# Optimization experiments

Measured on AMD Instinct MI355X. Metric: run time of the kernel, lower is better.

Reference implementation:

```python
import jax, jax.numpy as jnp
import numpy as np

N_NODES = 500_000
N_OUTDIM = 256
HIDDEN = 512
N_REPRE = 128
NUM_GRAPHS = 1024  # = max(graph_idx) + 1 by construction


def setup_inputs() -> dict:
    key = jax.random.key(0)
    ks = jax.random.split(key, 8)
    node_states = jax.random.normal(ks[0], (N_NODES, N_OUTDIM), dtype=jnp.float32)
    graph_idx = jnp.sort(jax.random.randint(ks[1], (N_NODES,), 0, NUM_GRAPHS, dtype=jnp.int64))
    s1 = 1.0 / np.sqrt(N_OUTDIM)
    s2 = 1.0 / np.sqrt(HIDDEN)
    W1 = jax.random.uniform(ks[2], (N_OUTDIM, HIDDEN), jnp.float32, -s1, s1)
    b1 = jax.random.uniform(ks[3], (HIDDEN,), jnp.float32, -s1, s1)
    W2 = jax.random.uniform(ks[4], (HIDDEN, HIDDEN), jnp.float32, -s2, s2)
    b2 = jax.random.uniform(ks[5], (HIDDEN,), jnp.float32, -s2, s2)
    W3 = jax.random.uniform(ks[6], (HIDDEN, N_REPRE), jnp.float32, -s2, s2)
    b3 = jax.random.uniform(ks[7], (N_REPRE,), jnp.float32, -s2, s2)
    return {"node_states": node_states, "graph_idx": graph_idx,
            "W1": W1, "b1": b1, "W2": W2, "b2": b2, "W3": W3, "b3": b3}


def reference(node_states, graph_idx, W1, b1, W2, b2, W3, b3):
    # 3-layer MLP: Linear -> ReLU -> Linear -> ReLU -> Linear
    h = jax.nn.relu(node_states @ W1 + b1)          # [N, HIDDEN]
    h = jax.nn.relu(h @ W2 + b2)                     # [N, HIDDEN]
    y = h @ W3 + b3                                  # [N, N_REPRE]
    # gated = sigmoid(y) * y  (SiLU)
    g = jax.nn.sigmoid(y) * y
    # scatter-add per-graph segment sum -> [NUM_GRAPHS, N_REPRE]
    return jax.ops.segment_sum(g, graph_idx, num_segments=NUM_GRAPHS)
```

## Files before the change

### kernel.cpp

```cpp
#include <hip/hip_runtime.h>
#include <stdint.h>


typedef short bf16x8 __attribute__((ext_vector_type(8)));
typedef float f32x4  __attribute__((ext_vector_type(4)));

#define N_NODES   500000
#define BM        32
#define N_BLOCKS  (N_NODES / BM)
#define N_GRAPHS  1024
#define N_OUT     128

#define W1P_ELEMS (256*512)
#define W2P_ELEMS (512*512)
#define W3P_ELEMS (512*128)
#define W2P_OFF   (W1P_ELEMS)
#define W3P_OFF   (W1P_ELEMS + W2P_ELEMS)
#define PREPACK_THREADS ((W1P_ELEMS + W2P_ELEMS + W3P_ELEMS) / 8)

__device__ __forceinline__ short f2bf(float x) {
    uint32_t u = __float_as_uint(x);
    u += 0x7fffu + ((u >> 16) & 1u);
    return (short)(u >> 16);
}

__global__ void prepack_weights(const float* __restrict__ W1,
                                const float* __restrict__ W2,
                                const float* __restrict__ W3,
                                short* __restrict__ wp) {
    int tid = blockIdx.x * blockDim.x + threadIdx.x;
    if (tid >= PREPACK_THREADS) return;
    const float* src; int N, kmask, kshift, dstoff, local;
    if (tid < 16384) {
        src = W1; N = 512; kmask = 7;  kshift = 3; dstoff = 0;       local = tid;
    } else if (tid < 49152) {
        src = W2; N = 512; kmask = 15; kshift = 4; dstoff = W2P_OFF; local = tid - 16384;
    } else {
        src = W3; N = 128; kmask = 15; kshift = 4; dstoff = W3P_OFF; local = tid - 49152;
    }
    const int lane = local & 63;
    const int tile = local >> 6;
    const int kt = tile & kmask;
    const int nt = tile >> kshift;
    const int k0 = kt * 32 + (lane >> 4) * 8;
    const int n  = nt * 16 + (lane & 15);
    const float* s = src + (size_t)k0 * N + n;
    union { bf16x8 v; short e[8]; } u;
#pragma unroll
    for (int j = 0; j < 8; ++j) u.e[j] = f2bf(s[(size_t)j * N]);
    *((bf16x8*)(wp + dstoff) + local) = u.v;
}

__launch_bounds__(256, 2)
__global__ void fused_mlp(const float* __restrict__ X,
                          const int*   __restrict__ gidx,
                          const short* __restrict__ wp,
                          const float* __restrict__ b1,
                          const float* __restrict__ b2,
                          const float* __restrict__ b3,
                          float* __restrict__ out) {
    __shared__ __align__(16) char lds[65536];
    char* R0 = lds;
    char* R1 = lds + 32768;

    const int t    = threadIdx.x;
    const int lane = t & 63;
    const int wave = t >> 6;
    const int q    = lane >> 4;
    const int l15  = lane & 15;
    const int64_t rowBase = (int64_t)blockIdx.x * BM;

    const f32x4 zero4 = {0.f, 0.f, 0.f, 0.f};

    {
        const int m  = t >> 3;
        const int s  = t & 7;
        const int sw = m & 7;
        const float* xr = X + (rowBase + m) * 256;
#pragma unroll
        for (int i = 0; i < 8; ++i) {
            const int col = (s + 8 * i) * 4;
            const float4 f = *(const float4*)(xr + col);
            short4 h;
            h.x = f2bf(f.x); h.y = f2bf(f.y); h.z = f2bf(f.z); h.w = f2bf(f.w);
            const int c = col >> 3;
            const int off = m * 512 + ((c ^ sw) << 4) + ((col >> 2) & 1) * 8;
            *(short4*)(R0 + off) = h;
        }
    }
    __syncthreads();

    {
        f32x4 acc[2][8];
#pragma unroll
        for (int rt = 0; rt < 2; ++rt)
#pragma unroll
            for (int c8 = 0; c8 < 8; ++c8) acc[rt][c8] = zero4;
        const bf16x8* wB = (const bf16x8*)wp;
        for (int kt = 0; kt < 8; ++kt) {
            bf16x8 a[2];
#pragma unroll
            for (int rt = 0; rt < 2; ++rt) {
                const int m = rt * 16 + l15;
                const int c = kt * 4 + q;
                a[rt] = *(const bf16x8*)(R0 + m * 512 + ((c ^ (m & 7)) << 4));
            }
#pragma unroll
            for (int c8 = 0; c8 < 8; ++c8) {
                const int ct = wave * 8 + c8;
                const bf16x8 b = wB[(ct * 8 + kt) * 64 + lane];
                acc[0][c8] = __builtin_amdgcn_mfma_f32_16x16x32_bf16(a[0], b, acc[0][c8], 0, 0, 0);
                acc[1][c8] = __builtin_amdgcn_mfma_f32_16x16x32_bf16(a[1], b, acc[1][c8], 0, 0, 0);
            }
        }
#pragma unroll
        for (int c8 = 0; c8 < 8; ++c8) {
            const int n = (wave * 8 + c8) * 16 + l15;
            const float bias = b1[n];
            const int cg = n >> 3;
            const int nl = n & 7;
#pragma unroll
            for (int rt = 0; rt < 2; ++rt)
#pragma unroll
                for (int r = 0; r < 4; ++r) {
                    const int m = rt * 16 + q * 4 + r;
                    float v = acc[rt][c8][r] + bias;
                    v = fmaxf(v, 0.f);
                    *(short*)(R1 + m * 1024 + ((cg ^ (m & 7)) << 4) + nl * 2) = f2bf(v);
                }
        }
    }
    __syncthreads();

    {
        f32x4 acc[2][8];
#pragma unroll
        for (int rt = 0; rt < 2; ++rt)
#pragma unroll
            for (int c8 = 0; c8 < 8; ++c8) acc[rt][c8] = zero4;
        const bf16x8* wB = (const bf16x8*)wp + (W2P_OFF >> 3);
        for (int kt = 0; kt < 16; ++kt) {
            bf16x8 a[2];
#pragma unroll
            for (int rt = 0; rt < 2; ++rt) {
                const int m = rt * 16 + l15;
                const int c = kt * 4 + q;
                a[rt] = *(const bf16x8*)(R1 + m * 1024 + ((c ^ (m & 7)) << 4));
            }
#pragma unroll
            for (int c8 = 0; c8 < 8; ++c8) {
                const int ct = wave * 8 + c8;
                const bf16x8 b = wB[(ct * 16 + kt) * 64 + lane];
                acc[0][c8] = __builtin_amdgcn_mfma_f32_16x16x32_bf16(a[0], b, acc[0][c8], 0, 0, 0);
                acc[1][c8] = __builtin_amdgcn_mfma_f32_16x16x32_bf16(a[1], b, acc[1][c8], 0, 0, 0);
            }
        }
#pragma unroll
        for (int c8 = 0; c8 < 8; ++c8) {
            const int n = (wave * 8 + c8) * 16 + l15;
            const float bias = b2[n];
            const int cg = n >> 3;
            const int nl = n & 7;
#pragma unroll
            for (int rt = 0; rt < 2; ++rt)
#pragma unroll
                for (int r = 0; r < 4; ++r) {
                    const int m = rt * 16 + q * 4 + r;
                    float v = acc[rt][c8][r] + bias;
                    v = fmaxf(v, 0.f);
                    *(short*)(R0 + m * 1024 + ((cg ^ (m & 7)) << 4) + nl * 2) = f2bf(v);
                }
        }
    }
    __syncthreads();

    {
        f32x4 acc[2][2];
#pragma unroll
        for (int rt = 0; rt < 2; ++rt)
#pragma unroll
            for (int c2 = 0; c2 < 2; ++c2) acc[rt][c2] = zero4;
        const bf16x8* wB = (const bf16x8*)wp + (W3P_OFF >> 3);
        for (int kt = 0; kt < 16; ++kt) {
            bf16x8 a[2];
#pragma unroll
            for (int rt = 0; rt < 2; ++rt) {
                const int m = rt * 16 + l15;
                const int c = kt * 4 + q;
                a[rt] = *(const bf16x8*)(R0 + m * 1024 + ((c ^ (m & 7)) << 4));
            }
#pragma unroll
            for (int c2 = 0; c2 < 2; ++c2) {
                const int ct = wave * 2 + c2;
                const bf16x8 b = wB[(ct * 16 + kt) * 64 + lane];
                acc[0][c2] = __builtin_amdgcn_mfma_f32_16x16x32_bf16(a[0], b, acc[0][c2], 0, 0, 0);
                acc[1][c2] = __builtin_amdgcn_mfma_f32_16x16x32_bf16(a[1], b, acc[1][c2], 0, 0, 0);
            }
        }
        float* yl = (float*)R1;
#pragma unroll
        for (int c2 = 0; c2 < 2; ++c2) {
            const int n = (wave * 2 + c2) * 16 + l15;
            const float bias = b3[n];
#pragma unroll
            for (int rt = 0; rt < 2; ++rt)
#pragma unroll
                for (int r = 0; r < 4; ++r) {
                    const int m = rt * 16 + q * 4 + r;
                    const float yv = acc[rt][c2][r] + bias;
                    const float gv = yv / (1.f + __expf(-yv));
                    yl[m * 132 + n] = gv;
                }
        }
    }
    __syncthreads();

    {
        int* gs = (int*)R0;
        if (t < BM) gs[t] = gidx[rowBase + t];
        __syncthreads();
        const int col = t & 127;
        const int r0  = (t >> 7) * 16;
        const float* yl = (const float*)R1;
        int   gprev = gs[r0];
        float acc   = 0.f;
        for (int r = r0; r < r0 + 16; ++r) {
            const int gr = gs[r];
            if (gr != gprev) {
                atomicAdd(out + gprev * N_OUT + col, acc);
                acc = 0.f;
                gprev = gr;
            }
            acc += yl[r * 132 + col];
        }
        atomicAdd(out + gprev * N_OUT + col, acc);
    }
}

extern "C" void kernel_launch(void* const* d_in, const int* in_sizes, int n_in,
                              void* d_out, int out_size, void* d_ws, size_t ws_size,
                              hipStream_t stream) {
    const float* X    = (const float*)d_in[0];
    const int*   gidx = (const int*)  d_in[1];
    const float* W1   = (const float*)d_in[2];
    const float* b1   = (const float*)d_in[3];
    const float* W2   = (const float*)d_in[4];
    const float* b2   = (const float*)d_in[5];
    const float* W3   = (const float*)d_in[6];
    const float* b3   = (const float*)d_in[7];
    float* out = (float*)d_out;
    short* wp  = (short*)d_ws;

    hipMemsetAsync(d_out, 0, sizeof(float) * N_GRAPHS * N_OUT, stream);

    prepack_weights<<<PREPACK_THREADS / 256, 256, 0, stream>>>(W1, W2, W3, wp);

    fused_mlp<<<N_BLOCKS, 256, 0, stream>>>(X, gidx, wp, b1, b2, b3, out);
}
```

Before: 1.189 ms.

## Double row tile to 64 with 8 waves and re-tiled weight layout

Raises the per-block row tile from 32 to 64 rows and the block from 256 to 512 threads. Each wave now computes 4 row tiles by 4 column tiles, so every weight fragment loaded from global memory feeds more MFMAs and total weight traffic per node drops. The weight prepack is reordered so the N-tiles for one K-step are contiguous, the MFMA operands are swapped so each lane holds four consecutive output columns, and bf16 conversion uses packed v_cvt_pk_bf16_f32 with vectorised epilogue stores. LDS use doubles to 128 KB per block and a tail guard is added for the partial last block, which may limit occupancy and adds bounds checks.

```diff
diff --git a/kernel.cpp b/kernel.cpp
--- a/kernel.cpp
+++ b/kernel.cpp
@@ -6,8 +6,8 @@
 typedef float f32x4  __attribute__((ext_vector_type(4)));
 
 #define N_NODES   500000
-#define BM        32
-#define N_BLOCKS  (N_NODES / BM)
+#define BM        64
+#define N_BLOCKS  ((N_NODES + BM - 1) / BM)
 #define N_GRAPHS  1024
 #define N_OUT     128
 
@@ -24,24 +24,30 @@
     return (short)(u >> 16);
 }
 
+__device__ __forceinline__ uint32_t pk2(float lo, float hi) {
+    uint32_t r;
+    asm("v_cvt_pk_bf16_f32 %0, %1, %2" : "=v"(r) : "v"(lo), "v"(hi));
+    return r;
+}
+
 __global__ void prepack_weights(const float* __restrict__ W1,
                                 const float* __restrict__ W2,
                                 const float* __restrict__ W3,
                                 short* __restrict__ wp) {
     int tid = blockIdx.x * blockDim.x + threadIdx.x;
     if (tid >= PREPACK_THREADS) return;
-    const float* src; int N, kmask, kshift, dstoff, local;
+    const float* src; int N, ntmask, ntshift, dstoff, local;
     if (tid < 16384) {
-        src = W1; N = 512; kmask = 7;  kshift = 3; dstoff = 0;       local = tid;
+        src = W1; N = 512; ntmask = 31; ntshift = 5; dstoff = 0;       local = tid;
     } else if (tid < 49152) {
-        src = W2; N = 512; kmask = 15; kshift = 4; dstoff = W2P_OFF; local = tid - 16384;
+        src = W2; N = 512; ntmask = 31; ntshift = 5; dstoff = W2P_OFF; local = tid - 16384;
     } else {
-        src = W3; N = 128; kmask = 15; kshift = 4; dstoff = W3P_OFF; local = tid - 49152;
+        src = W3; N = 128; ntmask = 7;  ntshift = 3; dstoff = W3P_OFF; local = tid - 49152;
     }
     const int lane = local & 63;
-    const int tile = local >> 6;
-    const int kt = tile & kmask;
-    const int nt = tile >> kshift;
+    const int f  = local >> 6;
+    const int nt = f & ntmask;
+    const int kt = f >> ntshift;
     const int k0 = kt * 32 + (lane >> 4) * 8;
     const int n  = nt * 16 + (lane & 15);
     const float* s = src + (size_t)k0 * N + n;
@@ -51,7 +57,7 @@
     *((bf16x8*)(wp + dstoff) + local) = u.v;
 }
 
-__launch_bounds__(256, 2)
+__launch_bounds__(512, 2)
 __global__ void fused_mlp(const float* __restrict__ X,
                           const int*   __restrict__ gidx,
                           const short* __restrict__ wp,
@@ -59,9 +65,9 @@
                           const float* __restrict__ b2,
                           const float* __restrict__ b3,
                           float* __restrict__ out) {
-    __shared__ __align__(16) char lds[65536];
+    __shared__ __align__(16) char lds[131072];
     char* R0 = lds;
-    char* R1 = lds + 32768;
+    char* R1 = lds + 65536;
 
     const int t    = threadIdx.x;
     const int lane = t & 63;
@@ -69,6 +75,8 @@
     const int q    = lane >> 4;
     const int l15  = lane & 15;
     const int64_t rowBase = (int64_t)blockIdx.x * BM;
+    int rowsValid = N_NODES - (int)rowBase;
+    if (rowsValid > BM) rowsValid = BM;
 
     const f32x4 zero4 = {0.f, 0.f, 0.f, 0.f};
 
@@ -76,164 +84,175 @@
         const int m  = t >> 3;
         const int s  = t & 7;
         const int sw = m & 7;
+        const bool valid = ((int)rowBase + m) < N_NODES;
         const float* xr = X + (rowBase + m) * 256;
 #pragma unroll
         for (int i = 0; i < 8; ++i) {
             const int col = (s + 8 * i) * 4;
-            const float4 f = *(const float4*)(xr + col);
-            short4 h;
-            h.x = f2bf(f.x); h.y = f2bf(f.y); h.z = f2bf(f.z); h.w = f2bf(f.w);
+            uint2 w; w.x = 0u; w.y = 0u;
+            if (valid) {
+                const float4 f = *(const float4*)(xr + col);
+                w.x = pk2(f.x, f.y);
+                w.y = pk2(f.z, f.w);
+            }
             const int c = col >> 3;
             const int off = m * 512 + ((c ^ sw) << 4) + ((col >> 2) & 1) * 8;
-            *(short4*)(R0 + off) = h;
-        }
-    }
-    __syncthreads();
-
-    {
-        f32x4 acc[2][8];
-#pragma unroll
-        for (int rt = 0; rt < 2; ++rt)
-#pragma unroll
-            for (int c8 = 0; c8 < 8; ++c8) acc[rt][c8] = zero4;
+            *(uint2*)(R0 + off) = w;
+        }
+    }
+    __syncthreads();
+
+    {
+        f32x4 acc[4][4];
+#pragma unroll
+        for (int rt = 0; rt < 4; ++rt)
+#pragma unroll
+            for (int c = 0; c < 4; ++c) acc[rt][c] = zero4;
         const bf16x8* wB = (const bf16x8*)wp;
+#pragma unroll 2
         for (int kt = 0; kt < 8; ++kt) {
-            bf16x8 a[2];
-#pragma unroll
-            for (int rt = 0; rt < 2; ++rt) {
-                const int m = rt * 16 + l15;
-                const int c = kt * 4 + q;
-                a[rt] = *(const bf16x8*)(R0 + m * 512 + ((c ^ (m & 7)) << 4));
-            }
-#pragma unroll
-            for (int c8 = 0; c8 < 8; ++c8) {
-                const int ct = wave * 8 + c8;
-                const bf16x8 b = wB[(ct * 8 + kt) * 64 + lane];
-                acc[0][c8] = __builtin_amdgcn_mfma_f32_16x16x32_bf16(a[0], b, acc[0][c8], 0, 0, 0);
-                acc[1][c8] = __builtin_amdgcn_mfma_f32_16x16x32_bf16(a[1], b, acc[1][c8], 0, 0, 0);
-            }
-        }
-#pragma unroll
-        for (int c8 = 0; c8 < 8; ++c8) {
-            const int n = (wave * 8 + c8) * 16 + l15;
-            const float bias = b1[n];
-            const int cg = n >> 3;
-            const int nl = n & 7;
-#pragma unroll
-            for (int rt = 0; rt < 2; ++rt)
-#pragma unroll
-                for (int r = 0; r < 4; ++r) {
-                    const int m = rt * 16 + q * 4 + r;
-                    float v = acc[rt][c8][r] + bias;
-                    v = fmaxf(v, 0.f);
-                    *(short*)(R1 + m * 1024 + ((cg ^ (m & 7)) << 4) + nl * 2) = f2bf(v);
-                }
-        }
-    }
-    __syncthreads();
-
-    {
-        f32x4 acc[2][8];
-#pragma unroll
-        for (int rt = 0; rt < 2; ++rt)
-#pragma unroll
-            for (int c8 = 0; c8 < 8; ++c8) acc[rt][c8] = zero4;
+            bf16x8 a[4];
+#pragma unroll
+            for (int rt = 0; rt < 4; ++rt) {
+                const int m = rt * 16 + l15;
+                a[rt] = *(const bf16x8*)(R0 + m * 512 + (((kt * 4 + q) ^ (m & 7)) << 4));
+            }
+            const bf16x8* bp = wB + ((kt * 32 + wave * 4) * 64 + lane);
+#pragma unroll
+            for (int c = 0; c < 4; ++c) {
+                const bf16x8 b = bp[c * 64];
+#pragma unroll
+                for (int rt = 0; rt < 4; ++rt)
+                    acc[rt][c] = __builtin_amdgcn_mfma_f32_16x16x32_bf16(b, a[rt], acc[rt][c], 0, 0, 0);
+            }
+        }
+#pragma unroll
+        for (int c = 0; c < 4; ++c) {
+            const int n0 = (wave * 4 + c) * 16 + q * 4;
+            const float4 bb = *(const float4*)(b1 + n0);
+            const int cg = n0 >> 3;
+            const int hb = (n0 & 7) << 1;
+#pragma unroll
+            for (int rt = 0; rt < 4; ++rt) {
+                const int m = rt * 16 + l15;
+                const float v0 = fmaxf(acc[rt][c][0] + bb.x, 0.f);
+                const float v1 = fmaxf(acc[rt][c][1] + bb.y, 0.f);
+                const float v2 = fmaxf(acc[rt][c][2] + bb.z, 0.f);
+                const float v3 = fmaxf(acc[rt][c][3] + bb.w, 0.f);
+                uint2 w; w.x = pk2(v0, v1); w.y = pk2(v2, v3);
+                *(uint2*)(R1 + m * 1024 + ((cg ^ (m & 7)) << 4) + hb) = w;
+            }
+        }
+    }
+    __syncthreads();
+
+    {
+        f32x4 acc[4][4];
+#pragma unroll
+        for (int rt = 0; rt < 4; ++rt)
+#pragma unroll
+            for (int c = 0; c < 4; ++c) acc[rt][c] = zero4;
         const bf16x8* wB = (const bf16x8*)wp + (W2P_OFF >> 3);
+#pragma unroll 2
         for (int kt = 0; kt < 16; ++kt) {
-            bf16x8 a[2];
-#pragma unroll
-            for (int rt = 0; rt < 2; ++rt) {
-                const int m = rt * 16 + l15;
-                const int c = kt * 4 + q;
-                a[rt] = *(const bf16x8*)(R1 + m * 1024 + ((c ^ (m & 7)) << 4));
-            }
-#pragma unroll
-            for (int c8 = 0; c8 < 8; ++c8) {
-                const int ct = wave * 8 + c8;
-                const bf16x8 b = wB[(ct * 16 + kt) * 64 + lane];
-                acc[0][c8] = __builtin_amdgcn_mfma_f32_16x16x32_bf16(a[0], b, acc[0][c8], 0, 0, 0);
-                acc[1][c8] = __builtin_amdgcn_mfma_f32_16x16x32_bf16(a[1], b, acc[1][c8], 0, 0, 0);
-            }
-        }
-#pragma unroll
-        for (int c8 = 0; c8 < 8; ++c8) {
-            const int n = (wave * 8 + c8) * 16 + l15;
-            const float bias = b2[n];
-            const int cg = n >> 3;
-            const int nl = n & 7;
-#pragma unroll
-            for (int rt = 0; rt < 2; ++rt)
-#pragma unroll
-                for (int r = 0; r < 4; ++r) {
-                    const int m = rt * 16 + q * 4 + r;
-                    float v = acc[rt][c8][r] + bias;
-                    v = fmaxf(v, 0.f);
-                    *(short*)(R0 + m * 1024 + ((cg ^ (m & 7)) << 4) + nl * 2) = f2bf(v);
-                }
-        }
-    }
-    __syncthreads();
-
-    {
-        f32x4 acc[2][2];
-#pragma unroll
-        for (int rt = 0; rt < 2; ++rt)
-#pragma unroll
-            for (int c2 = 0; c2 < 2; ++c2) acc[rt][c2] = zero4;
+            bf16x8 a[4];
+#pragma unroll
+            for (int rt = 0; rt < 4; ++rt) {
+                const int m = rt * 16 + l15;
+                a[rt] = *(const bf16x8*)(R1 + m * 1024 + (((kt * 4 + q) ^ (m & 7)) << 4));
+            }
+            const bf16x8* bp = wB + ((kt * 32 + wave * 4) * 64 + lane);
+#pragma unroll
+            for (int c = 0; c < 4; ++c) {
+                const bf16x8 b = bp[c * 64];
+#pragma unroll
+                for (int rt = 0; rt < 4; ++rt)
+                    acc[rt][c] = __builtin_amdgcn_mfma_f32_16x16x32_bf16(b, a[rt], acc[rt][c], 0, 0, 0);
+            }
+        }
+#pragma unroll
+        for (int c = 0; c < 4; ++c) {
+            const int n0 = (wave * 4 + c) * 16 + q * 4;
+            const float4 bb = *(const float4*)(b2 + n0);
+            const int cg = n0 >> 3;
+            const int hb = (n0 & 7) << 1;
+#pragma unroll
+            for (int rt = 0; rt < 4; ++rt) {
+                const int m = rt * 16 + l15;
+                const float v0 = fmaxf(acc[rt][c][0] + bb.x, 0.f);
+                const float v1 = fmaxf(acc[rt][c][1] + bb.y, 0.f);
+                const float v2 = fmaxf(acc[rt][c][2] + bb.z, 0.f);
+                const float v3 = fmaxf(acc[rt][c][3] + bb.w, 0.f);
+                uint2 w; w.x = pk2(v0, v1); w.y = pk2(v2, v3);
+                *(uint2*)(R0 + m * 1024 + ((cg ^ (m & 7)) << 4) + hb) = w;
+            }
+        }
+    }
+    __syncthreads();
+
+    {
+        f32x4 acc[4];
+#pragma unroll
+        for (int rt = 0; rt < 4; ++rt) acc[rt] = zero4;
         const bf16x8* wB = (const bf16x8*)wp + (W3P_OFF >> 3);
         for (int kt = 0; kt < 16; ++kt) {
-            bf16x8 a[2];
-#pragma unroll
-            for (int rt = 0; rt < 2; ++rt) {
-                const int m = rt * 16 + l15;
-                const int c = kt * 4 + q;
-                a[rt] = *(const bf16x8*)(R0 + m * 1024 + ((c ^ (m & 7)) << 4));
-            }
-#pragma unroll
-            for (int c2 = 0; c2 < 2; ++c2) {
-                const int ct = wave * 2 + c2;
-                const bf16x8 b = wB[(ct * 16 + kt) * 64 + lane];
-                acc[0][c2] = __builtin_amdgcn_mfma_f32_16x16x32_bf16(a[0], b, acc[0][c2], 0, 0, 0);
-                acc[1][c2] = __builtin_amdgcn_mfma_f32_16x16x32_bf16(a[1], b, acc[1][c2], 0, 0, 0);
-            }
+            bf16x8 a[4];
+#pragma unroll
+            for (int rt = 0; rt < 4; ++rt) {
+                const int m = rt * 16 + l15;
+                a[rt] = *(const bf16x8*)(R0 + m * 1024 + (((kt * 4 + q) ^ (m & 7)) << 4));
+            }
+            const bf16x8 b = wB[(kt * 8 + wave) * 64 + lane];
+#pragma unroll
+            for (int rt = 0; rt < 4; ++rt)
+                acc[rt] = __builtin_amdgcn_mfma_f32_16x16x32_bf16(b, a[rt], acc[rt], 0, 0, 0);
         }
         float* yl = (float*)R1;
-#pragma unroll
-        for (int c2 = 0; c2 < 2; ++c2) {
-            const int n = (wave * 2 + c2) * 16 + l15;
-            const float bias = b3[n];
-#pragma unroll
-            for (int rt = 0; rt < 2; ++rt)
-#pragma unroll
-                for (int r = 0; r < 4; ++r) {
-                    const int m = rt * 16 + q * 4 + r;
-                    const float yv = acc[rt][c2][r] + bias;
-                    const float gv = yv / (1.f + __expf(-yv));
-                    yl[m * 132 + n] = gv;
-                }
+        const int n0 = wave * 16 + q * 4;
+        const float4 bb = *(const float4*)(b3 + n0);
+#pragma unroll
+        for (int rt = 0; rt < 4; ++rt) {
+            const int m = rt * 16 + l15;
+            const float y0 = acc[rt][0] + bb.x;
+            const float y1 = acc[rt][1] + bb.y;
+            const float y2 = acc[rt][2] + bb.z;
+            const float y3 = acc[rt][3] + bb.w;
+            float4 o;
+            o.x = y0 / (1.f + __expf(-y0));
+            o.y = y1 / (1.f + __expf(-y1));
+            o.z = y2 / (1.f + __expf(-y2));
+            o.w = y3 / (1.f + __expf(-y3));
+            *(float4*)(yl + m * 132 + n0) = o;
         }
     }
     __syncthreads();
 
     {
         int* gs = (int*)R0;
-        if (t < BM) gs[t] = gidx[rowBase + t];
+        if (t < BM) {
+            const int r = (int)rowBase + t;
+            gs[t] = (r < N_NODES) ? gidx[r] : 0;
+        }
         __syncthreads();
         const int col = t & 127;
         const int r0  = (t >> 7) * 16;
-        const float* yl = (const float*)R1;
-        int   gprev = gs[r0];
-        float acc   = 0.f;
-        for (int r = r0; r < r0 + 16; ++r) {
-            const int gr = gs[r];
-            if (gr != gprev) {
-                atomicAdd(out + gprev * N_OUT + col, acc);
-                acc = 0.f;
-                gprev = gr;
-            }
-            acc += yl[r * 132 + col];
-        }
-        atomicAdd(out + gprev * N_OUT + col, acc);
+        int rend = r0 + 16;
+        if (rend > rowsValid) rend = rowsValid;
+        if (r0 < rend) {
+            const float* yl = (const float*)R1;
+            int   gprev = gs[r0];
+            float acc   = 0.f;
+            for (int r = r0; r < rend; ++r) {
+                const int gr = gs[r];
+                if (gr != gprev) {
+                    atomicAdd(out + gprev * N_OUT + col, acc);
+                    acc = 0.f;
+                    gprev = gr;
+                }
+                acc += yl[r * 132 + col];
+            }
+            atomicAdd(out + gprev * N_OUT + col, acc);
+        }
     }
 }
 
@@ -255,5 +274,5 @@
 
     prepack_weights<<<PREPACK_THREADS / 256, 256, 0, stream>>>(W1, W2, W3, wp);
 
-    fused_mlp<<<N_BLOCKS, 256, 0, stream>>>(X, gidx, wp, b1, b2, b3, out);
-}
+    fused_mlp<<<N_BLOCKS, 512, 0, stream>>>(X, gidx, wp, b1, b2, b3, out);
+}
```

Measured after the change: 1.306 ms. 9.8% more time.
